# Optimization experiments

Measured on AMD Instinct MI355X. Metric: run time of the kernel, lower is better.

Reference implementation:

```python
import jax, jax.numpy as jnp
import numpy as np

B, S, D = 16, 577, 768      # batch, BLIP vision tokens (1 CLS + 576 patches), hidden
C, NCLS = 256, 1000         # num_concepts, num_classes
TOPK = 16


def setup_inputs() -> dict:
    key = jax.random.key(0)
    k1, k2, k3 = jax.random.split(key, 3)
    q = jax.random.normal(k1, (B, S, D), dtype=jnp.float32)          # BLIP last_hidden_state
    concept_w = jax.random.normal(k2, (C, D), dtype=jnp.float32) * 0.02  # nn.Embedding weight
    cls_w = jax.random.normal(k3, (NCLS, D), dtype=jnp.float32) * 0.02   # nn.Linear weight
    cls_b = jnp.zeros((NCLS,), dtype=jnp.float32)
    return {"q": q, "concept_w": concept_w, "cls_w": cls_w, "cls_b": cls_b, "topk": TOPK}


def reference(q, concept_w, cls_w, cls_b, topk):
    qp = q[:, 1:]                                             # [B, S-1, D] drop CLS token
    qk = jnp.einsum('bsd,cd->bcs', qp, concept_w)             # [B, C, S-1] concept similarities
    qk_topk, idx_topk = jax.lax.top_k(qk, topk)               # [B, C, K]
    # batched gather: q_topk[b,c,k] = qp[b, idx_topk[b,c,k]]
    q_topk = jnp.take_along_axis(qp[:, None], idx_topk[..., None], axis=2)  # [B, C, K, D]
    score = jax.nn.softmax(qk_topk, axis=2)                   # [B, C, K]
    h = (q_topk * score[..., None]).sum(axis=2).mean(axis=1)  # [B, D]
    y = jax.nn.relu(h) @ cls_w.T + cls_b                      # [B, NCLS]
    return y
```

## Files before the change

### kernel.cpp

```cpp
#include <hip/hip_runtime.h>

#define NB 16
#define S_TOK 577
#define SP 576
#define DIM 768
#define NC 256
#define NCLS 1000
#define TK 16
#define HCH 6
#define HCHS 96

typedef __attribute__((ext_vector_type(8))) __bf16 bf16x8;
typedef __attribute__((ext_vector_type(4))) float f32x4;

__device__ __forceinline__ void cvt_split(const float4 a, const float4 b,
                                          bf16x8& hi, bf16x8& lo) {
  float v[8] = {a.x, a.y, a.z, a.w, b.x, b.y, b.z, b.w};
#pragma unroll
  for (int i = 0; i < 8; i++) {
    __bf16 h = (__bf16)v[i];
    hi[i] = h;
    lo[i] = (__bf16)(v[i] - (float)h);
  }
}

__device__ __forceinline__ bf16x8 frag_ld(const char* base, int r, int kc) {
  return *(const bf16x8*)(base + ((r * 4 + (kc ^ (r & 3))) << 4));
}

__global__ __launch_bounds__(256) void qk_gemm_mfma(const float* __restrict__ q,
                                                    const float* __restrict__ cw,
                                                    float* __restrict__ qk,
                                                    float* __restrict__ W, int b0) {
  const int bl = blockIdx.z;
  const int s0 = blockIdx.x * 64;
  const int c0 = blockIdx.y * 128;
  __shared__ __align__(16) char sAH[8192], sAL[8192], sBH[4096], sBL[4096];

  if (blockIdx.x == 0 && blockIdx.y == 0) {
    for (int i = threadIdx.x; i < SP; i += 256) W[(b0 + bl) * SP + i] = 0.f;
  }

  const int tid = threadIdx.x;
  const int lane = tid & 63;
  const int wid = tid >> 6;
  const int wc = (wid >> 1) << 6;
  const int wsv = (wid & 1) << 5;
  const int fr = lane & 15;
  const int kq = lane >> 4;

  const int ra0 = (tid * 2) >> 2, cka0 = (tid * 2) & 3;
  const int ra1 = (tid * 2 + 1) >> 2, cka1 = (tid * 2 + 1) & 3;
  const int rb = tid >> 2, ckb = tid & 3;
  const int slotA0 = (ra0 * 4 + (cka0 ^ (ra0 & 3))) << 4;
  const int slotA1 = (ra1 * 4 + (cka1 ^ (ra1 & 3))) << 4;
  const int slotB = (rb * 4 + (ckb ^ (rb & 3))) << 4;

  const float* qb = q + ((size_t)(b0 + bl) * S_TOK + 1) * DIM;
  const float* arow0 = cw + (size_t)(c0 + ra0) * DIM + cka0 * 8;
  const float* arow1 = cw + (size_t)(c0 + ra1) * DIM + cka1 * 8;
  const float* brow = qb + (size_t)(s0 + rb) * DIM + ckb * 8;

  f32x4 zero = {0.f, 0.f, 0.f, 0.f};
  f32x4 acc[4][2];
#pragma unroll
  for (int i = 0; i < 4; i++)
#pragma unroll
    for (int j = 0; j < 2; j++) acc[i][j] = zero;

  for (int k0 = 0; k0 < DIM; k0 += 32) {
    float4 a00 = *(const float4*)(arow0 + k0);
    float4 a01 = *(const float4*)(arow0 + k0 + 4);
    float4 a10 = *(const float4*)(arow1 + k0);
    float4 a11 = *(const float4*)(arow1 + k0 + 4);
    float4 b0v = *(const float4*)(brow + k0);
    float4 b1v = *(const float4*)(brow + k0 + 4);
    __syncthreads();
    bf16x8 h, l;
    cvt_split(a00, a01, h, l);
    *(bf16x8*)(sAH + slotA0) = h;
    *(bf16x8*)(sAL + slotA0) = l;
    cvt_split(a10, a11, h, l);
    *(bf16x8*)(sAH + slotA1) = h;
    *(bf16x8*)(sAL + slotA1) = l;
    cvt_split(b0v, b1v, h, l);
    *(bf16x8*)(sBH + slotB) = h;
    *(bf16x8*)(sBL + slotB) = l;
    __syncthreads();
    bf16x8 ah[4], al[4], bh[2], blo[2];
#pragma unroll
    for (int i = 0; i < 4; i++) {
      ah[i] = frag_ld(sAH, wc + i * 16 + fr, kq);
      al[i] = frag_ld(sAL, wc + i * 16 + fr, kq);
    }
#pragma unroll
    for (int j = 0; j < 2; j++) {
      bh[j] = frag_ld(sBH, wsv + j * 16 + fr, kq);
      blo[j] = frag_ld(sBL, wsv + j * 16 + fr, kq);
    }
#define MF(A, B, C) C = __builtin_amdgcn_mfma_f32_16x16x32_bf16(A, B, C, 0, 0, 0)
#pragma unroll
    for (int i = 0; i < 4; i++)
#pragma unroll
      for (int j = 0; j < 2; j++) {
        MF(ah[i], bh[j], acc[i][j]);
        MF(ah[i], blo[j], acc[i][j]);
        MF(al[i], bh[j], acc[i][j]);
      }
#undef MF
  }
  float* obase = qk + (size_t)bl * NC * SP;
#pragma unroll
  for (int i = 0; i < 4; i++)
#pragma unroll
    for (int j = 0; j < 2; j++)
#pragma unroll
      for (int rr = 0; rr < 4; rr++) {
        const int row = c0 + wc + i * 16 + kq * 4 + rr;
        const int col = s0 + wsv + j * 16 + fr;
        obase[(size_t)row * SP + col] = acc[i][j][rr];
      }
}

__global__ __launch_bounds__(256) void topk_scatter(const float* __restrict__ qk,
                                                    float* __restrict__ W, int b0) {
  const int lane = threadIdx.x & 63;
  const int wid = threadIdx.x >> 6;
  const int rcl = blockIdx.x * 4 + wid;
  const int bl = rcl >> 8;
  const int b = b0 + bl;
  const float* rowp = qk + (size_t)rcl * SP;
  float v[9];
#pragma unroll
  for (int j = 0; j < 9; j++) v[j] = rowp[lane + 64 * j];

  float vals[TK];
  int idxs[TK];
#pragma unroll
  for (int t = 0; t < TK; t++) {
    float bv = -1e30f;
    int bj = 0;
#pragma unroll
    for (int j = 0; j < 9; j++)
      if (v[j] > bv) { bv = v[j]; bj = j; }
    int bs = lane + 64 * bj;
#pragma unroll
    for (int off = 32; off >= 1; off >>= 1) {
      float ov = __shfl_xor(bv, off);
      int os = __shfl_xor(bs, off);
      if (ov > bv || (ov == bv && os < bs)) { bv = ov; bs = os; }
    }
    vals[t] = bv;
    idxs[t] = bs;
    const int clr_j = bs >> 6;
    const int clr_lane = bs & 63;
#pragma unroll
    for (int j = 0; j < 9; j++)
      if (j == clr_j && clr_lane == lane) v[j] = -1e30f;
  }
  float m = vals[0];
  float sum = 0.f;
#pragma unroll
  for (int t = 0; t < TK; t++) sum += expf(vals[t] - m);
  if (lane == 0) {
    const float inv = 1.f / (sum * (float)NC);
#pragma unroll
    for (int t = 0; t < TK; t++)
      atomicAdd(&W[b * SP + idxs[t]], expf(vals[t] - m) * inv);
  }
}

__global__ __launch_bounds__(256) void h_partial(const float* __restrict__ q,
                                                 const float* __restrict__ W,
                                                 float* __restrict__ hpart) {
  const int b = blockIdx.y;
  const int ch = blockIdx.z;
  const int d = blockIdx.x * 256 + threadIdx.x;
  __shared__ float Ws[HCHS];
  if (threadIdx.x < HCHS) Ws[threadIdx.x] = W[b * SP + ch * HCHS + threadIdx.x];
  __syncthreads();
  const float* qb = q + ((size_t)b * S_TOK + 1 + ch * HCHS) * DIM + d;
  float acc = 0.f;
#pragma unroll 8
  for (int s = 0; s < HCHS; s++) acc = fmaf(Ws[s], qb[(size_t)s * DIM], acc);
  hpart[((size_t)ch * NB + b) * DIM + d] = acc;
}

__global__ __launch_bounds__(256) void cls_head(const float* __restrict__ hp,
                                                const float* __restrict__ cw,
                                                const float* __restrict__ cb,
                                                float* __restrict__ y) {
  __shared__ float hs[NB * DIM];
  for (int i = threadIdx.x; i < NB * DIM; i += 256) {
    float s = 0.f;
#pragma unroll
    for (int ch = 0; ch < HCH; ch++) s += hp[(size_t)ch * NB * DIM + i];
    hs[i] = fmaxf(s, 0.f);
  }
  __syncthreads();
  const int lane = threadIdx.x & 63;
  const int n = blockIdx.x * 4 + (threadIdx.x >> 6);
  float wr[12];
#pragma unroll
  for (int j = 0; j < 12; j++) wr[j] = cw[(size_t)n * DIM + lane + 64 * j];
  const float bias = cb[n];
  for (int bb = 0; bb < NB; bb++) {
    float dot = 0.f;
#pragma unroll
    for (int j = 0; j < 12; j++)
      dot = fmaf(wr[j], hs[bb * DIM + lane + 64 * j], dot);
#pragma unroll
    for (int off = 32; off >= 1; off >>= 1) dot += __shfl_xor(dot, off);
    if (lane == 0) y[bb * NCLS + n] = dot + bias;
  }
}

extern "C" void kernel_launch(void* const* d_in, const int* in_sizes, int n_in,
                              void* d_out, int out_size, void* d_ws, size_t ws_size,
                              hipStream_t stream) {
  const float* q = (const float*)d_in[0];
  const float* cw = (const float*)d_in[1];
  const float* clsw = (const float*)d_in[2];
  const float* clsb = (const float*)d_in[3];
  float* out = (float*)d_out;

  float* W = (float*)d_ws;
  float* hpart = W + (size_t)NB * SP;
  float* qk = hpart + (size_t)HCH * NB * DIM;
  const size_t aux_bytes = (size_t)((char*)qk - (char*)d_ws);

  int bper = NB;
  while (bper > 1 &&
         aux_bytes + (size_t)bper * NC * SP * sizeof(float) > ws_size)
    bper >>= 1;

  for (int b0 = 0; b0 < NB; b0 += bper) {
    qk_gemm_mfma<<<dim3(9, 2, bper), 256, 0, stream>>>(q, cw, qk, W, b0);
    topk_scatter<<<(bper * NC) / 4, 256, 0, stream>>>(qk, W, b0);
  }
  h_partial<<<dim3(3, NB, HCH), 256, 0, stream>>>(q, W, hpart);
  cls_head<<<NCLS / 4, 256, 0, stream>>>(hpart, clsw, clsb, out);
}
```

Measured before the change: 73.88 us.

## Pre-split inputs to bf16 hi/lo in separate pass and retile qk GEMM

Adds a conversion kernel that splits q and the concept weights into bf16 hi/lo buffers in workspace once, so the GEMM no longer redoes the fp32-to-bf16 split for every tile. The GEMM is retiled to 64x144 blocks with a 64-wide K step, wider 8-chunk XOR swizzle, and register prefetch of the next K tile overlapping MFMA work. The cost is an extra pass writing about 28MB of bf16 data, which the GEMM then reads back, and fewer blocks (4x4 per batch) with larger LDS use.

```diff
diff --git a/kernel.cpp b/kernel.cpp
--- a/kernel.cpp
+++ b/kernel.cpp
@@ -13,113 +13,148 @@
 typedef __attribute__((ext_vector_type(8))) __bf16 bf16x8;
 typedef __attribute__((ext_vector_type(4))) float f32x4;
 
-__device__ __forceinline__ void cvt_split(const float4 a, const float4 b,
-                                          bf16x8& hi, bf16x8& lo) {
-  float v[8] = {a.x, a.y, a.z, a.w, b.x, b.y, b.z, b.w};
+__global__ __launch_bounds__(256) void cvt_split_k(const float* __restrict__ q,
+                                                   const float* __restrict__ cw,
+                                                   __bf16* __restrict__ qph,
+                                                   __bf16* __restrict__ qpl,
+                                                   __bf16* __restrict__ cwh,
+                                                   __bf16* __restrict__ cwl,
+                                                   float* __restrict__ W) {
+  const int gid = blockIdx.x * 256 + threadIdx.x;
+  if (gid < NB * SP) W[gid] = 0.f;
+  const int QCH = NB * SP * (DIM / 8);
+  const float* src;
+  __bf16 *dh, *dl;
+  if (gid < QCH) {
+    const int rid = gid / (DIM / 8);
+    const int kc = gid % (DIM / 8);
+    const int b = rid / SP, s = rid % SP;
+    src = q + (((size_t)b * S_TOK + 1 + s) * DIM + kc * 8);
+    dh = qph + ((size_t)rid * DIM + kc * 8);
+    dl = qpl + ((size_t)rid * DIM + kc * 8);
+  } else {
+    const int cid = gid - QCH;
+    src = cw + (size_t)cid * 8;
+    dh = cwh + (size_t)cid * 8;
+    dl = cwl + (size_t)cid * 8;
+  }
+  float4 v0 = *(const float4*)src;
+  float4 v1 = *(const float4*)(src + 4);
+  float v[8] = {v0.x, v0.y, v0.z, v0.w, v1.x, v1.y, v1.z, v1.w};
+  bf16x8 h, l;
 #pragma unroll
   for (int i = 0; i < 8; i++) {
-    __bf16 h = (__bf16)v[i];
-    hi[i] = h;
-    lo[i] = (__bf16)(v[i] - (float)h);
-  }
-}
-
-__device__ __forceinline__ bf16x8 frag_ld(const char* base, int r, int kc) {
-  return *(const bf16x8*)(base + ((r * 4 + (kc ^ (r & 3))) << 4));
-}
-
-__global__ __launch_bounds__(256) void qk_gemm_mfma(const float* __restrict__ q,
-                                                    const float* __restrict__ cw,
-                                                    float* __restrict__ qk,
-                                                    float* __restrict__ W, int b0) {
+    __bf16 hh = (__bf16)v[i];
+    h[i] = hh;
+    l[i] = (__bf16)(v[i] - (float)hh);
+  }
+  *(bf16x8*)dh = h;
+  *(bf16x8*)dl = l;
+}
+
+__global__ __launch_bounds__(256) void qk_gemm_bf16(const __bf16* __restrict__ qph,
+                                                    const __bf16* __restrict__ qpl,
+                                                    const __bf16* __restrict__ cwh,
+                                                    const __bf16* __restrict__ cwl,
+                                                    float* __restrict__ qk, int b0) {
   const int bl = blockIdx.z;
-  const int s0 = blockIdx.x * 64;
-  const int c0 = blockIdx.y * 128;
-  __shared__ __align__(16) char sAH[8192], sAL[8192], sBH[4096], sBL[4096];
-
-  if (blockIdx.x == 0 && blockIdx.y == 0) {
-    for (int i = threadIdx.x; i < SP; i += 256) W[(b0 + bl) * SP + i] = 0.f;
-  }
+  const int b = b0 + bl;
+  const int s0 = blockIdx.x * 144;
+  const int c0 = blockIdx.y * 64;
+  __shared__ __align__(16) __bf16 sAH[64 * 64], sAL[64 * 64];
+  __shared__ __align__(16) __bf16 sBH[144 * 64], sBL[144 * 64];
 
   const int tid = threadIdx.x;
   const int lane = tid & 63;
   const int wid = tid >> 6;
-  const int wc = (wid >> 1) << 6;
-  const int wsv = (wid & 1) << 5;
+  const int wc = wid << 4;
   const int fr = lane & 15;
-  const int kq = lane >> 4;
-
-  const int ra0 = (tid * 2) >> 2, cka0 = (tid * 2) & 3;
-  const int ra1 = (tid * 2 + 1) >> 2, cka1 = (tid * 2 + 1) & 3;
-  const int rb = tid >> 2, ckb = tid & 3;
-  const int slotA0 = (ra0 * 4 + (cka0 ^ (ra0 & 3))) << 4;
-  const int slotA1 = (ra1 * 4 + (cka1 ^ (ra1 & 3))) << 4;
-  const int slotB = (rb * 4 + (ckb ^ (rb & 3))) << 4;
-
-  const float* qb = q + ((size_t)(b0 + bl) * S_TOK + 1) * DIM;
-  const float* arow0 = cw + (size_t)(c0 + ra0) * DIM + cka0 * 8;
-  const float* arow1 = cw + (size_t)(c0 + ra1) * DIM + cka1 * 8;
-  const float* brow = qb + (size_t)(s0 + rb) * DIM + ckb * 8;
-
-  f32x4 zero = {0.f, 0.f, 0.f, 0.f};
-  f32x4 acc[4][2];
-#pragma unroll
-  for (int i = 0; i < 4; i++)
-#pragma unroll
-    for (int j = 0; j < 2; j++) acc[i][j] = zero;
-
-  for (int k0 = 0; k0 < DIM; k0 += 32) {
-    float4 a00 = *(const float4*)(arow0 + k0);
-    float4 a01 = *(const float4*)(arow0 + k0 + 4);
-    float4 a10 = *(const float4*)(arow1 + k0);
-    float4 a11 = *(const float4*)(arow1 + k0 + 4);
-    float4 b0v = *(const float4*)(brow + k0);
-    float4 b1v = *(const float4*)(brow + k0 + 4);
+  const int kqm = lane >> 4;
+  const int frs = fr & 7;
+
+  const int rb = tid >> 3;
+  const int kc = tid & 7;
+  const int slw = (kc ^ (rb & 7)) * 8;
+
+  const __bf16* qbh = qph + (size_t)b * SP * DIM;
+  const __bf16* qbl = qpl + (size_t)b * SP * DIM;
+
+  f32x4 acc[9];
+#pragma unroll
+  for (int j = 0; j < 9; j++) acc[j] = (f32x4){0.f, 0.f, 0.f, 0.f};
+
+  bf16x8 rAh[2], rAl[2], rBh[5], rBl[5];
+
+#define LOADREGS(K0)                                                          \
+  {                                                                           \
+    const int k0_ = (K0);                                                     \
+    _Pragma("unroll") for (int m = 0; m < 2; ++m) {                           \
+      const size_t g = (size_t)(c0 + m * 32 + rb) * DIM + k0_ + kc * 8;       \
+      rAh[m] = *(const bf16x8*)(cwh + g);                                     \
+      rAl[m] = *(const bf16x8*)(cwl + g);                                     \
+    }                                                                         \
+    _Pragma("unroll") for (int m = 0; m < 4; ++m) {                           \
+      const size_t g = (size_t)(s0 + m * 32 + rb) * DIM + k0_ + kc * 8;       \
+      rBh[m] = *(const bf16x8*)(qbh + g);                                     \
+      rBl[m] = *(const bf16x8*)(qbl + g);                                     \
+    }                                                                         \
+    if (tid < 128) {                                                          \
+      const size_t g = (size_t)(s0 + 128 + rb) * DIM + k0_ + kc * 8;          \
+      rBh[4] = *(const bf16x8*)(qbh + g);                                     \
+      rBl[4] = *(const bf16x8*)(qbl + g);                                     \
+    }                                                                         \
+  }
+
+  LOADREGS(0);
+  for (int kt = 0; kt < 12; ++kt) {
     __syncthreads();
-    bf16x8 h, l;
-    cvt_split(a00, a01, h, l);
-    *(bf16x8*)(sAH + slotA0) = h;
-    *(bf16x8*)(sAL + slotA0) = l;
-    cvt_split(a10, a11, h, l);
-    *(bf16x8*)(sAH + slotA1) = h;
-    *(bf16x8*)(sAL + slotA1) = l;
-    cvt_split(b0v, b1v, h, l);
-    *(bf16x8*)(sBH + slotB) = h;
-    *(bf16x8*)(sBL + slotB) = l;
+#pragma unroll
+    for (int m = 0; m < 2; ++m) {
+      const int r = m * 32 + rb;
+      *(bf16x8*)(sAH + r * 64 + slw) = rAh[m];
+      *(bf16x8*)(sAL + r * 64 + slw) = rAl[m];
+    }
+#pragma unroll
+    for (int m = 0; m < 4; ++m) {
+      const int r = m * 32 + rb;
+      *(bf16x8*)(sBH + r * 64 + slw) = rBh[m];
+      *(bf16x8*)(sBL + r * 64 + slw) = rBl[m];
+    }
+    if (tid < 128) {
+      const int r = 128 + rb;
+      *(bf16x8*)(sBH + r * 64 + slw) = rBh[4];
+      *(bf16x8*)(sBL + r * 64 + slw) = rBl[4];
+    }
     __syncthreads();
-    bf16x8 ah[4], al[4], bh[2], blo[2];
-#pragma unroll
-    for (int i = 0; i < 4; i++) {
-      ah[i] = frag_ld(sAH, wc + i * 16 + fr, kq);
-      al[i] = frag_ld(sAL, wc + i * 16 + fr, kq);
-    }
-#pragma unroll
-    for (int j = 0; j < 2; j++) {
-      bh[j] = frag_ld(sBH, wsv + j * 16 + fr, kq);
-      blo[j] = frag_ld(sBL, wsv + j * 16 + fr, kq);
-    }
+    if (kt < 11) LOADREGS((kt + 1) * 64);
 #define MF(A, B, C) C = __builtin_amdgcn_mfma_f32_16x16x32_bf16(A, B, C, 0, 0, 0)
 #pragma unroll
-    for (int i = 0; i < 4; i++)
-#pragma unroll
-      for (int j = 0; j < 2; j++) {
-        MF(ah[i], bh[j], acc[i][j]);
-        MF(ah[i], blo[j], acc[i][j]);
-        MF(al[i], bh[j], acc[i][j]);
+    for (int ks = 0; ks < 2; ++ks) {
+      const int sl = ((ks * 4 + kqm) ^ frs) * 8;
+      const bf16x8 ah = *(const bf16x8*)(sAH + (wc + fr) * 64 + sl);
+      const bf16x8 al = *(const bf16x8*)(sAL + (wc + fr) * 64 + sl);
+#pragma unroll
+      for (int j = 0; j < 9; ++j) {
+        const int br = j * 16 + fr;
+        const bf16x8 bh = *(const bf16x8*)(sBH + br * 64 + sl);
+        const bf16x8 bv = *(const bf16x8*)(sBL + br * 64 + sl);
+        MF(ah, bh, acc[j]);
+        MF(ah, bv, acc[j]);
+        MF(al, bh, acc[j]);
       }
+    }
 #undef MF
   }
+#undef LOADREGS
   float* obase = qk + (size_t)bl * NC * SP;
 #pragma unroll
-  for (int i = 0; i < 4; i++)
-#pragma unroll
-    for (int j = 0; j < 2; j++)
-#pragma unroll
-      for (int rr = 0; rr < 4; rr++) {
-        const int row = c0 + wc + i * 16 + kq * 4 + rr;
-        const int col = s0 + wsv + j * 16 + fr;
-        obase[(size_t)row * SP + col] = acc[i][j][rr];
-      }
+  for (int j = 0; j < 9; ++j)
+#pragma unroll
+    for (int rr = 0; rr < 4; ++rr) {
+      const int row = c0 + wc + kqm * 4 + rr;
+      const int col = s0 + j * 16 + fr;
+      obase[(size_t)row * SP + col] = acc[j][rr];
+    }
 }
 
 __global__ __launch_bounds__(256) void topk_scatter(const float* __restrict__ qk,
@@ -224,7 +259,11 @@
   const float* clsb = (const float*)d_in[3];
   float* out = (float*)d_out;
 
-  float* W = (float*)d_ws;
+  __bf16* qph = (__bf16*)d_ws;
+  __bf16* qpl = qph + (size_t)NB * SP * DIM;
+  __bf16* cwh = qpl + (size_t)NB * SP * DIM;
+  __bf16* cwl = cwh + (size_t)NC * DIM;
+  float* W = (float*)(cwl + (size_t)NC * DIM);
   float* hpart = W + (size_t)NB * SP;
   float* qk = hpart + (size_t)HCH * NB * DIM;
   const size_t aux_bytes = (size_t)((char*)qk - (char*)d_ws);
@@ -234,8 +273,11 @@
          aux_bytes + (size_t)bper * NC * SP * sizeof(float) > ws_size)
     bper >>= 1;
 
+  const int CVT_BLOCKS = (NB * SP * (DIM / 8) + NC * (DIM / 8)) / 256;
+  cvt_split_k<<<CVT_BLOCKS, 256, 0, stream>>>(q, cw, qph, qpl, cwh, cwl, W);
+
   for (int b0 = 0; b0 < NB; b0 += bper) {
-    qk_gemm_mfma<<<dim3(9, 2, bper), 256, 0, stream>>>(q, cw, qk, W, b0);
+    qk_gemm_bf16<<<dim3(4, 4, bper), 256, 0, stream>>>(qph, qpl, cwh, cwl, qk, b0);
     topk_scatter<<<(bper * NC) / 4, 256, 0, stream>>>(qk, W, b0);
   }
   h_partial<<<dim3(3, NB, HCH), 256, 0, stream>>>(q, W, hpart);
```

Measured after the change: 81.99 us. 1.11x slower.
